# Optimization experiments

Hardware: AMD Instinct MI355X
Metric: run time of the kernel (lower is better)

Reference implementation:

```python
import jax, jax.numpy as jnp
import numpy as np

RESO = 256          # grid resolution per axis
BASIS_DIM = 9       # SH basis dim -> sh channels = 27
N_PTS = 2_000_000   # number of sample points
RADIUS = 1.0


def _build_links():
    # Replicates SparseGrid.__init__ sphere-bound link construction (static, numpy).
    g = np.arange(RESO, dtype=np.float32) - 0.5
    X, Y, Z = np.meshgrid(g, g, g, indexing='ij')
    pts = np.stack([X, Y, Z], axis=-1).reshape(-1, 3)
    roffset = 1.0 / RESO - 1.0
    rscaling = 2.0 / RESO
    pts = roffset + pts * rscaling
    norms = np.linalg.norm(pts, axis=-1)
    mask = norms <= 1.0 + (3.0 ** 0.5) / RESO
    links = np.full(RESO ** 3, -1, dtype=np.int32)
    links[mask] = np.arange(int(mask.sum()), dtype=np.int32)
    return links.reshape(RESO, RESO, RESO), int(mask.sum())


_CORNERS = np.array([[dx, dy, dz] for dx in (0, 1) for dy in (0, 1) for dz in (0, 1)],
                    dtype=np.float32)  # [8,3]


def setup_inputs() -> dict:
    key = jax.random.key(0)
    k1, k2, k3 = jax.random.split(key, 3)
    links_np, capacity = _build_links()
    links = jnp.asarray(links_np)
    density_data = 0.1 * jax.random.normal(k1, (capacity, 1), dtype=jnp.float32)
    sh_data = 0.1 * jax.random.normal(k2, (capacity, BASIS_DIM * 3), dtype=jnp.float32)
    # world-space points uniformly in the grid AABB [-radius, radius]
    points = jax.random.uniform(k3, (N_PTS, 3), dtype=jnp.float32,
                                minval=-RADIUS, maxval=RADIUS)
    return {"points": points, "density_data": density_data,
            "sh_data": sh_data, "links": links}


def _sample(points, density_data, sh_data, links):
    gsz = links.shape[0]  # cubic grid
    # world->grid: _offset=0.5*(1-c/r)=0.5, _scaling=0.5/r; cpp: off*gsz-0.5, scl*gsz
    scaling = (0.5 / RADIUS) * gsz
    offset = 0.5 * gsz - 0.5
    pos = points * scaling + offset
    pos = jnp.clip(pos, 0.0, gsz - 1.0)
    l = jnp.clip(jnp.floor(pos), 0.0, gsz - 2.0)
    t = pos - l                      # [N,3] in [0,1]
    l = l.astype(jnp.int32)
    flat_links = links.reshape(-1)
    base = (l[:, 0] * gsz + l[:, 1]) * gsz + l[:, 2]          # [N]
    corners = jnp.asarray(_CORNERS)                            # [8,3]
    corner_off = (_CORNERS[:, 0] * gsz * gsz + _CORNERS[:, 1] * gsz
                  + _CORNERS[:, 2]).astype(np.int32)
    idx = base[:, None] + jnp.asarray(corner_off)[None, :]     # [N,8]
    lnk = jnp.take(flat_links, idx)                            # [N,8] sparse link gather
    safe = jnp.maximum(lnk, 0)
    valid = (lnk >= 0)[:, :, None]
    # trilinear weights: prod over axes of (t or 1-t)
    w = jnp.prod(corners[None] * t[:, None, :] + (1.0 - corners[None]) * (1.0 - t[:, None, :]),
                 axis=-1)                                      # [N,8]
    out_density = jnp.zeros((points.shape[0], 1), jnp.float32)
    out_sh = jnp.zeros((points.shape[0], BASIS_DIM * 3), jnp.float32)
    for c in range(8):  # fixed small corner loop avoids [N,8,27] intermediate
        lc = safe[:, c]
        vmask = valid[:, c]
        wc = w[:, c:c + 1]
        out_density = out_density + wc * jnp.where(vmask, density_data[lc], 0.0)
        out_sh = out_sh + wc * jnp.where(vmask, sh_data[lc], 0.0)
    return out_density, out_sh


def reference(points, density_data, sh_data, links):
    return _sample(points, density_data, sh_data, links)
```

## Files before the change

### kernel.cpp

```cpp
#include <hip/hip_runtime.h>

#define RESO 256
#define NCH 27
#define PTS_PER_BLK 32
#define ITEMS (PTS_PER_BLK * 28)

__global__ __launch_bounds__(256) void sg_sample_kernel(
    const float* __restrict__ points,
    const float* __restrict__ dens,
    const float* __restrict__ sh,
    const int*   __restrict__ links,
    float* __restrict__ out_d,
    float* __restrict__ out_sh,
    int n)
{
    __shared__ float s_w[PTS_PER_BLK][8];
    __shared__ int   s_addr[PTS_PER_BLK][8];
    __shared__ float s_wd[PTS_PER_BLK][8];

    const int tid = threadIdx.x;
    const int pl  = tid >> 3;
    const int c   = tid & 7;
    const int pg  = blockIdx.x * PTS_PER_BLK + pl;

    if (pg < n) {
        const float px = points[3*pg+0];
        const float py = points[3*pg+1];
        const float pz = points[3*pg+2];

        const float posx = fminf(fmaxf(px*128.0f + 127.5f, 0.0f), 255.0f);
        const float posy = fminf(fmaxf(py*128.0f + 127.5f, 0.0f), 255.0f);
        const float posz = fminf(fmaxf(pz*128.0f + 127.5f, 0.0f), 255.0f);
        const float lxf = fminf(floorf(posx), 254.0f);
        const float lyf = fminf(floorf(posy), 254.0f);
        const float lzf = fminf(floorf(posz), 254.0f);
        const float tx = posx - lxf;
        const float ty = posy - lyf;
        const float tz = posz - lzf;
        const int base = ((int)lxf << 16) | ((int)lyf << 8) | (int)lzf;
        const int off  = ((c & 4) << 14) + ((c & 2) << 7) + (c & 1);

        const int lnk = links[base + off];

        const float wx = (c & 4) ? tx : 1.0f - tx;
        const float wy = (c & 2) ? ty : 1.0f - ty;
        const float wz = (c & 1) ? tz : 1.0f - tz;
        const float w  = (wx * wy) * wz;

        const int   safe = (lnk >= 0) ? lnk : 0;
        const float wv   = (lnk >= 0) ? w : 0.0f;
        s_w[pl][c]    = wv;
        s_addr[pl][c] = safe * NCH;
        s_wd[pl][c]   = wv * dens[safe];
    } else {
        s_w[pl][c]    = 0.0f;
        s_addr[pl][c] = 0;
        s_wd[pl][c]   = 0.0f;
    }
    __syncthreads();

    const int base_pt = blockIdx.x * PTS_PER_BLK;

    float vals[4][8];
    int   pp[4], jj[4];

    #pragma unroll
    for (int u = 0; u < 4; ++u) {
        const int item = tid + u * 256;
        const int it   = (item < ITEMS) ? item : 0;
        const int p = it / 28;
        const int j = it - p * 28;
        pp[u] = p; jj[u] = j;
        const int q = (j == 0) ? 0 : j - 1;
        #pragma unroll
        for (int cc = 0; cc < 8; ++cc) {
            vals[u][cc] = sh[s_addr[p][cc] + q];
        }
    }

    #pragma unroll
    for (int u = 0; u < 4; ++u) {
        const int item = tid + u * 256;
        if (item >= ITEMS) continue;
        const int p = pp[u], j = jj[u];
        const int pg2 = base_pt + p;
        if (pg2 >= n) continue;
        if (j == 0) {
            float a = 0.0f;
            #pragma unroll
            for (int cc = 0; cc < 8; ++cc) a += s_wd[p][cc];
            out_d[pg2] = a;
        } else {
            float acc0 = 0.0f, acc1 = 0.0f;
            #pragma unroll
            for (int cc = 0; cc < 8; cc += 2) {
                acc0 += s_w[p][cc]     * vals[u][cc];
                acc1 += s_w[p][cc + 1] * vals[u][cc + 1];
            }
            out_sh[pg2 * NCH + (j - 1)] = acc0 + acc1;
        }
    }
}

extern "C" void kernel_launch(void* const* d_in, const int* in_sizes, int n_in,
                              void* d_out, int out_size, void* d_ws, size_t ws_size,
                              hipStream_t stream) {
    const float* points = (const float*)d_in[0];
    const float* dens   = (const float*)d_in[1];
    const float* sh     = (const float*)d_in[2];
    const int*   links  = (const int*)d_in[3];
    const int n = in_sizes[0] / 3;

    float* out_d  = (float*)d_out;
    float* out_sh = out_d + n;

    const int grid = (n + PTS_PER_BLK - 1) / PTS_PER_BLK;
    hipLaunchKernelGGL(sg_sample_kernel, dim3(grid), dim3(256), 0, stream,
                       points, dens, sh, links, out_d, out_sh, n);
}
```

Before: 452.0 us.

## Bucket-sort points by coarse voxel before sampling to improve gather locality

Adds a counting sort of points into 32^3 coarse spatial buckets (histogram, single-block scan, atomic scatter). The sampling kernel then runs over the sorted points and writes results back through the permutation. The aim is better cache locality for the links and sh gathers. The cost is three extra kernels, a memset, and scattered output writes. It falls back to the original kernel when the workspace is too small.

```diff
diff --git a/kernel.cpp b/kernel.cpp
--- a/kernel.cpp
+++ b/kernel.cpp
@@ -4,9 +4,66 @@
 #define NCH 27
 #define PTS_PER_BLK 32
 #define ITEMS (PTS_PER_BLK * 28)
-
-__global__ __launch_bounds__(256) void sg_sample_kernel(
-    const float* __restrict__ points,
+#define NBUCKET 32768
+
+
+__global__ __launch_bounds__(256) void key_hist_kernel(
+    const float* __restrict__ pts, int* __restrict__ keys,
+    int* __restrict__ hist, int n)
+{
+    const int i = blockIdx.x * blockDim.x + threadIdx.x;
+    if (i >= n) return;
+    const float px = pts[3*i+0], py = pts[3*i+1], pz = pts[3*i+2];
+    const int ix = (int)fminf(fmaxf(px*128.0f + 127.5f, 0.0f), 255.0f);
+    const int iy = (int)fminf(fmaxf(py*128.0f + 127.5f, 0.0f), 255.0f);
+    const int iz = (int)fminf(fmaxf(pz*128.0f + 127.5f, 0.0f), 255.0f);
+    const int key = ((ix >> 3) << 10) | ((iy >> 3) << 5) | (iz >> 3);
+    keys[i] = key;
+    atomicAdd(&hist[key], 1);
+}
+
+__global__ __launch_bounds__(1024) void scan_hist_kernel(
+    const int* __restrict__ hist, int* __restrict__ offs)
+{
+    __shared__ int part[1024];
+    const int t = threadIdx.x;
+    const int base = t * 32;
+    int v[32];
+    int s = 0;
+    #pragma unroll
+    for (int k = 0; k < 32; ++k) { v[k] = hist[base + k]; s += v[k]; }
+    part[t] = s;
+    __syncthreads();
+    for (int off = 1; off < 1024; off <<= 1) {
+        const int x = (t >= off) ? part[t - off] : 0;
+        __syncthreads();
+        part[t] += x;
+        __syncthreads();
+    }
+    int run = part[t] - s;
+    #pragma unroll
+    for (int k = 0; k < 32; ++k) { offs[base + k] = run; run += v[k]; }
+}
+
+__global__ __launch_bounds__(256) void scatter_kernel(
+    const float* __restrict__ pts, const int* __restrict__ keys,
+    int* __restrict__ offs, int* __restrict__ perm,
+    float* __restrict__ spts, int n)
+{
+    const int i = blockIdx.x * blockDim.x + threadIdx.x;
+    if (i >= n) return;
+    const int key = keys[i];
+    const int pos = atomicAdd(&offs[key], 1);
+    perm[pos] = i;
+    spts[3*pos+0] = pts[3*i+0];
+    spts[3*pos+1] = pts[3*i+1];
+    spts[3*pos+2] = pts[3*i+2];
+}
+
+
+__global__ __launch_bounds__(256) void sg_sample_sorted_kernel(
+    const float* __restrict__ spts,
+    const int*   __restrict__ perm,
     const float* __restrict__ dens,
     const float* __restrict__ sh,
     const int*   __restrict__ links,
@@ -17,16 +74,17 @@
     __shared__ float s_w[PTS_PER_BLK][8];
     __shared__ int   s_addr[PTS_PER_BLK][8];
     __shared__ float s_wd[PTS_PER_BLK][8];
+    __shared__ int   s_orig[PTS_PER_BLK];
 
     const int tid = threadIdx.x;
     const int pl  = tid >> 3;
     const int c   = tid & 7;
-    const int pg  = blockIdx.x * PTS_PER_BLK + pl;
-
-    if (pg < n) {
-        const float px = points[3*pg+0];
-        const float py = points[3*pg+1];
-        const float pz = points[3*pg+2];
+    const int g   = blockIdx.x * PTS_PER_BLK + pl;
+
+    if (g < n) {
+        const float px = spts[3*g+0];
+        const float py = spts[3*g+1];
+        const float pz = spts[3*g+2];
 
         const float posx = fminf(fmaxf(px*128.0f + 127.5f, 0.0f), 255.0f);
         const float posy = fminf(fmaxf(py*128.0f + 127.5f, 0.0f), 255.0f);
@@ -52,10 +110,12 @@
         s_w[pl][c]    = wv;
         s_addr[pl][c] = safe * NCH;
         s_wd[pl][c]   = wv * dens[safe];
+        s_orig[pl]    = perm[g];
     } else {
         s_w[pl][c]    = 0.0f;
         s_addr[pl][c] = 0;
         s_wd[pl][c]   = 0.0f;
+        s_orig[pl]    = 0;
     }
     __syncthreads();
 
@@ -83,6 +143,93 @@
         const int item = tid + u * 256;
         if (item >= ITEMS) continue;
         const int p = pp[u], j = jj[u];
+        if (base_pt + p >= n) continue;
+        const int orig = s_orig[p];
+        if (j == 0) {
+            float a = 0.0f;
+            #pragma unroll
+            for (int cc = 0; cc < 8; ++cc) a += s_wd[p][cc];
+            out_d[orig] = a;
+        } else {
+            float acc0 = 0.0f, acc1 = 0.0f;
+            #pragma unroll
+            for (int cc = 0; cc < 8; cc += 2) {
+                acc0 += s_w[p][cc]     * vals[u][cc];
+                acc1 += s_w[p][cc + 1] * vals[u][cc + 1];
+            }
+            out_sh[orig * NCH + (j - 1)] = acc0 + acc1;
+        }
+    }
+}
+
+
+__global__ __launch_bounds__(256) void sg_sample_kernel(
+    const float* __restrict__ points,
+    const float* __restrict__ dens,
+    const float* __restrict__ sh,
+    const int*   __restrict__ links,
+    float* __restrict__ out_d,
+    float* __restrict__ out_sh,
+    int n)
+{
+    __shared__ float s_w[PTS_PER_BLK][8];
+    __shared__ int   s_addr[PTS_PER_BLK][8];
+    __shared__ float s_wd[PTS_PER_BLK][8];
+
+    const int tid = threadIdx.x;
+    const int pl  = tid >> 3;
+    const int c   = tid & 7;
+    const int pg  = blockIdx.x * PTS_PER_BLK + pl;
+
+    if (pg < n) {
+        const float px = points[3*pg+0];
+        const float py = points[3*pg+1];
+        const float pz = points[3*pg+2];
+        const float posx = fminf(fmaxf(px*128.0f + 127.5f, 0.0f), 255.0f);
+        const float posy = fminf(fmaxf(py*128.0f + 127.5f, 0.0f), 255.0f);
+        const float posz = fminf(fmaxf(pz*128.0f + 127.5f, 0.0f), 255.0f);
+        const float lxf = fminf(floorf(posx), 254.0f);
+        const float lyf = fminf(floorf(posy), 254.0f);
+        const float lzf = fminf(floorf(posz), 254.0f);
+        const float tx = posx - lxf, ty = posy - lyf, tz = posz - lzf;
+        const int base = ((int)lxf << 16) | ((int)lyf << 8) | (int)lzf;
+        const int off  = ((c & 4) << 14) + ((c & 2) << 7) + (c & 1);
+        const int lnk = links[base + off];
+        const float wx = (c & 4) ? tx : 1.0f - tx;
+        const float wy = (c & 2) ? ty : 1.0f - ty;
+        const float wz = (c & 1) ? tz : 1.0f - tz;
+        const float w  = (wx * wy) * wz;
+        const int   safe = (lnk >= 0) ? lnk : 0;
+        const float wv   = (lnk >= 0) ? w : 0.0f;
+        s_w[pl][c]    = wv;
+        s_addr[pl][c] = safe * NCH;
+        s_wd[pl][c]   = wv * dens[safe];
+    } else {
+        s_w[pl][c] = 0.0f; s_addr[pl][c] = 0; s_wd[pl][c] = 0.0f;
+    }
+    __syncthreads();
+
+    const int base_pt = blockIdx.x * PTS_PER_BLK;
+    float vals[4][8];
+    int   pp[4], jj[4];
+
+    #pragma unroll
+    for (int u = 0; u < 4; ++u) {
+        const int item = tid + u * 256;
+        const int it   = (item < ITEMS) ? item : 0;
+        const int p = it / 28;
+        const int j = it - p * 28;
+        pp[u] = p; jj[u] = j;
+        const int q = (j == 0) ? 0 : j - 1;
+        #pragma unroll
+        for (int cc = 0; cc < 8; ++cc) vals[u][cc] = sh[s_addr[p][cc] + q];
+    }
+
+    #pragma unroll
+    for (int u = 0; u < 4; ++u) {
+        const int item = tid + u * 256;
+        if (item >= ITEMS) continue;
+        const int p = pp[u], j = jj[u];
         const int pg2 = base_pt + p;
         if (pg2 >= n) continue;
         if (j == 0) {
@@ -101,6 +248,7 @@
         }
     }
 }
+
 
 extern "C" void kernel_launch(void* const* d_in, const int* in_sizes, int n_in,
                               void* d_out, int out_size, void* d_ws, size_t ws_size,
@@ -114,7 +262,32 @@
     float* out_d  = (float*)d_out;
     float* out_sh = out_d + n;
 
-    const int grid = (n + PTS_PER_BLK - 1) / PTS_PER_BLK;
-    hipLaunchKernelGGL(sg_sample_kernel, dim3(grid), dim3(256), 0, stream,
-                       points, dens, sh, links, out_d, out_sh, n);
-}
+    const size_t histB = (size_t)NBUCKET * 4;
+    const size_t need  = 2 * histB + (size_t)n * 4 * 2 + (size_t)n * 12;
+
+    if (ws_size >= need) {
+        char* ws = (char*)d_ws;
+        int*   hist = (int*)ws;
+        int*   offs = (int*)(ws + histB);
+        int*   keys = (int*)(ws + 2 * histB);
+        int*   perm = (int*)(ws + 2 * histB + (size_t)n * 4);
+        float* spts = (float*)(ws + 2 * histB + (size_t)n * 8);
+
+        hipMemsetAsync(hist, 0, histB, stream);
+
+        const int gridN = (n + 255) / 256;
+        hipLaunchKernelGGL(key_hist_kernel, dim3(gridN), dim3(256), 0, stream,
+                           points, keys, hist, n);
+        hipLaunchKernelGGL(scan_hist_kernel, dim3(1), dim3(1024), 0, stream,
+                           hist, offs);
+        hipLaunchKernelGGL(scatter_kernel, dim3(gridN), dim3(256), 0, stream,
+                           points, keys, offs, perm, spts, n);
+        const int gridS = (n + PTS_PER_BLK - 1) / PTS_PER_BLK;
+        hipLaunchKernelGGL(sg_sample_sorted_kernel, dim3(gridS), dim3(256), 0, stream,
+                           spts, perm, dens, sh, links, out_d, out_sh, n);
+    } else {
+        const int gridS = (n + PTS_PER_BLK - 1) / PTS_PER_BLK;
+        hipLaunchKernelGGL(sg_sample_kernel, dim3(gridS), dim3(256), 0, stream,
+                           points, dens, sh, links, out_d, out_sh, n);
+    }
+}
```

After: 628.5 us. 1.39x slower.
